# Kernel tuning notes

Measured on AMD Instinct MI355X. Metric: run time of the kernel, lower is better.

## Reference

```python
import jax, jax.numpy as jnp
import numpy as np

GRID = 33
STRIDE = 2
HIDDEN = 256
N_LAYERS = 4
BATCH = 64
N_NODES = GRID * GRID  # 1089


def _stride_edges(g, s):
    """Replicates StrideGraphSAGE.stride_edge (including the strict j > s test)."""
    idx = np.arange(g * g).reshape(g, g)
    srcs, dsts = [], []
    # right neighbor: j < g - s
    srcs.append(idx[:, : g - s].ravel()); dsts.append(idx[:, s:].ravel())
    # down neighbor: i < g - s
    srcs.append(idx[: g - s, :].ravel()); dsts.append(idx[s:, :].ravel())
    # down-right: j < g - s and i < g - s
    srcs.append(idx[: g - s, : g - s].ravel()); dsts.append(idx[s:, s:].ravel())
    # down-left: j > s and i < g - s  (strict >, as in the original)
    srcs.append(idx[: g - s, s + 1 :].ravel()); dsts.append(idx[s:, 1 : g - s].ravel())
    return (np.concatenate(srcs).astype(np.int32),
            np.concatenate(dsts).astype(np.int32))


def setup_inputs() -> dict:
    key = jax.random.key(0)
    kx, kwl, kbl, kwr = jax.random.split(key, 4)
    x = jax.random.normal(kx, (BATCH, HIDDEN, GRID, GRID), dtype=jnp.float32)
    Wl = jax.random.normal(kwl, (N_LAYERS, HIDDEN, HIDDEN), dtype=jnp.float32) * 0.05
    bl = jax.random.normal(kbl, (N_LAYERS, HIDDEN), dtype=jnp.float32) * 0.05
    Wr = jax.random.normal(kwr, (N_LAYERS, HIDDEN, HIDDEN), dtype=jnp.float32) * 0.05
    src_np, dst_np = _stride_edges(GRID, STRIDE)
    return {
        "x": x, "Wl": Wl, "bl": bl, "Wr": Wr,
        "src": jnp.asarray(src_np), "dst": jnp.asarray(dst_np),
    }


def reference(x, Wl, bl, Wr, src, dst):
    B, C, H, W = x.shape
    N = H * W
    total = B * N
    # feature2graph: each image -> [N, C] node matrix, then batched -> [B*N, C]
    nodes = x.reshape(B, C, N).transpose(0, 2, 1).reshape(total, C)

    # The original passes the UNOFFSET single-graph edge_index to every layer,
    # so messages only flow among the first N rows; the rest get zero aggregate.
    deg = jnp.zeros((total,), x.dtype).at[dst].add(1.0)
    inv_deg = jnp.where(deg > 0, 1.0 / jnp.maximum(deg, 1.0), 0.0)[:, None]

    L = Wl.shape[0]
    outs = []
    for l in range(L):
        # SAGEConv (mean aggr): lin_l(mean_j x_src_j) + lin_r(x) ; every layer
        # is applied to the ORIGINAL node features (x is never updated).
        agg = jnp.zeros_like(nodes).at[dst].add(nodes[src]) * inv_deg
        h = agg @ Wl[l] + bl[l] + nodes @ Wr[l]
        h = jax.nn.elu(h)
        # graph2feature: raw contiguous view [N, C] -> (C, H, W) per graph
        outs.append(h.reshape(B, C, H, W))
    outs.append(x)
    return jnp.concatenate(outs, axis=1)
```

## Files before the change

kernel.cpp:

```cpp
#include <hip/hip_runtime.h>
#include <hip/hip_bf16.h>
#include <stdint.h>


#define C_DIM 256
#define GRID_G 33
#define N_NODES 1089
#define BATCH 64
#define TOTAL (BATCH * N_NODES)
#define M_PAD 69760
#define CN (C_DIM * N_NODES)
#define OUT_STRIDE_B (5 * CN)
#define NCOLS 1024
#define AGG_ROWS_PAD 1280
#define MT 273
#define NWG (MT * 4)

using bf16 = __hip_bfloat16;
typedef __attribute__((ext_vector_type(8))) short short8;
typedef __attribute__((ext_vector_type(4))) float f32x4;

#define NODES_BYTES ((size_t)M_PAD * C_DIM * 2)
#define OFF_NODES   ((size_t)0)
#define OFF_AGGB    (NODES_BYTES)
#define AGGB_BYTES  ((size_t)AGG_ROWS_PAD * C_DIM * 2)
#define OFF_WLT     (OFF_AGGB + AGGB_BYTES)
#define WT_BYTES    ((size_t)NCOLS * C_DIM * 2)
#define OFF_WRT     (OFF_WLT + WT_BYTES)

__device__ __forceinline__ void gload16(void* lds, const void* g) {
    __builtin_amdgcn_global_load_lds(
        (const __attribute__((address_space(1))) uint32_t*)g,
        (__attribute__((address_space(3))) uint32_t*)lds,
        16, 0, 0);
}

__global__ __launch_bounds__(256)
void prep_kernel(const float* __restrict__ x,
                 const float* __restrict__ Wl, const float* __restrict__ Wr,
                 bf16* __restrict__ nodes, bf16* __restrict__ WlT, bf16* __restrict__ WrT,
                 float* __restrict__ out)
{
    __shared__ char smem[33792];
    const int t = threadIdx.x;
    const int bid = blockIdx.x;
    if (bid < 128) {
        float (*tile)[65] = (float(*)[65])smem;
        const int sel = bid & 1;
        const int l = (bid >> 1) & 3;
        const int kt = ((bid >> 3) & 3) * 64;
        const int ct = ((bid >> 5) & 3) * 64;
        const float* W = sel ? Wr : Wl;
        bf16* WT = sel ? WrT : WlT;
        const int tc = t & 63;
        const int tk = t >> 6;
#pragma unroll
        for (int i = 0; i < 16; ++i) {
            int kl = i * 4 + tk;
            tile[kl][tc] = W[((size_t)(l * 256 + kt + kl)) * 256 + ct + tc];
        }
        __syncthreads();
#pragma unroll
        for (int i = 0; i < 16; ++i) {
            int cl = i * 4 + tk;
            WT[((size_t)(l * 256 + ct + cl)) * 256 + kt + tc] = __float2bfloat16(tile[tc][cl]);
        }
    } else {
        bf16 (*tile)[66] = (bf16(*)[66])smem;
        const int bid2 = bid - 128;
        const int b = bid2 / 18;
        const int n0 = (bid2 % 18) * 64;
        const int nl = t & 63;
        const int cs = t >> 6;
        const int n = n0 + nl;
        const bool nvalid = n < N_NODES;
        const float* xb = x + (size_t)b * CN;
        float* outb = out + (size_t)b * OUT_STRIDE_B + (size_t)4 * CN;
#pragma unroll 4
        for (int cc = 0; cc < 64; ++cc) {
            int c = cc * 4 + cs;
            if (nvalid) {
                float v = xb[(size_t)c * N_NODES + n];
                outb[(size_t)c * N_NODES + n] = v;
                tile[c][nl] = __float2bfloat16(v);
            }
        }
        __syncthreads();
        const int half = t >> 7;
        const int c0 = (t & 127) * 2;
#pragma unroll
        for (int it = 0; it < 32; ++it) {
            int row = it * 2 + half;
            int nr = n0 + row;
            if (nr < N_NODES) {
                __hip_bfloat162 p;
                p.x = tile[c0][row];
                p.y = tile[c0 + 1][row];
                *(__hip_bfloat162*)(nodes + ((size_t)b * N_NODES + nr) * C_DIM + c0) = p;
            }
        }
    }
}

__global__ __launch_bounds__(256)
void gather_kernel(const bf16* __restrict__ nodes, bf16* __restrict__ aggb)
{
    const int n = blockIdx.x;
    const int c = threadIdx.x;
    if (n >= N_NODES) {
        aggb[(size_t)n * C_DIM + c] = __float2bfloat16(0.f);
        return;
    }
    const int i = n / GRID_G, j = n % GRID_G;
    float s = 0.f, d = 0.f;
    if (j >= 2)           { s += __bfloat162float(nodes[(size_t)(n - 2)  * C_DIM + c]); d += 1.f; }
    if (i >= 2)           { s += __bfloat162float(nodes[(size_t)(n - 66) * C_DIM + c]); d += 1.f; }
    if (i >= 2 && j >= 2) { s += __bfloat162float(nodes[(size_t)(n - 68) * C_DIM + c]); d += 1.f; }
    if (i >= 2 && j >= 1 && j <= 30)
                          { s += __bfloat162float(nodes[(size_t)(n - 64) * C_DIM + c]); d += 1.f; }
    aggb[(size_t)n * C_DIM + c] = __float2bfloat16(d > 0.f ? s / d : 0.f);
}

__global__ __launch_bounds__(512)
void gemm_kernel(const bf16* __restrict__ nodes, const bf16* __restrict__ agg,
                 const bf16* __restrict__ WrT, const bf16* __restrict__ WlT,
                 const float* __restrict__ bias, float* __restrict__ out)
{
    extern __shared__ char Sb[];
    const int t = threadIdx.x;
    const int lane = t & 63;
    const int w = t >> 6;
    const int wm = w >> 2;
    const int wn = w & 3;
    const int fr = lane & 15;
    const int kq = lane >> 4;

    const unsigned bid = blockIdx.x;
    const unsigned xcd = bid & 7, loc = bid >> 3;
    const unsigned swz = (xcd < 4 ? xcd * 137u : 4u * 137u + (xcd - 4u) * 136u) + loc;
    const int bcol = swz & 3;
    const int brow = swz >> 2;

    const int NT = (brow * 256 < N_NODES) ? 8 : 4;
    const size_t Arow0 = (size_t)brow * 256;
    const size_t Brow0 = (size_t)bcol * 256;

    f32x4 acc[8][4] = {};

    const int srow = t >> 3;
    const int sk = (((t & 7) ^ (srow & 7)) << 3);
    const int so0 = ((0 * 4 + kq) ^ (fr & 7)) << 4;
    const int so1 = ((1 * 4 + kq) ^ (fr & 7)) << 4;
    const int arow_b = (wm * 128 + fr) * 128;
    const int brow_b = (wn * 64 + fr) * 128;

    auto STAGE_HALF = [&](int kt, int half, int isB) {
        const int buf = kt & 1;
        const int kk0 = ((kt & 3) << 6) + sk;
        if (!isB) {
            const bf16* src = (kt < 4 ? nodes : agg);
            const size_t gr = Arow0 + half * 128 + srow;
            char* dst = Sb + buf * 32768 + half * 16384 + w * 1024;
            gload16(dst,        src + gr * 256 + kk0);
            gload16(dst + 8192, src + (gr + 64) * 256 + kk0);
        } else {
            const bf16* src = (kt < 4 ? WrT : WlT);
            const size_t gr = Brow0 + half * 128 + srow;
            char* dst = Sb + 65536 + buf * 32768 + half * 16384 + w * 1024;
            gload16(dst,        src + gr * 256 + kk0);
            gload16(dst + 8192, src + (gr + 64) * 256 + kk0);
        }
    };

    STAGE_HALF(0, 0, 0); STAGE_HALF(0, 1, 0); STAGE_HALF(0, 0, 1); STAGE_HALF(0, 1, 1);
    STAGE_HALF(1, 0, 0); STAGE_HALF(1, 1, 0); STAGE_HALF(1, 0, 1); STAGE_HALF(1, 1, 1);
    asm volatile("s_waitcnt vmcnt(8)" ::: "memory");
    __builtin_amdgcn_s_barrier();

    short8 av[4][2], bv0[2][2], bv1[2][2];

    for (int kt = 0; kt < NT; ++kt) {
        const int ab = (kt & 1) * 32768;
        const int bb = 65536 + (kt & 1) * 32768;
        const bool pf = (kt + 1 < NT);

#pragma unroll
        for (int i = 0; i < 4; ++i) {
            av[i][0] = *(const short8*)(Sb + ab + arow_b + i * 2048 + so0);
            av[i][1] = *(const short8*)(Sb + ab + arow_b + i * 2048 + so1);
        }
#pragma unroll
        for (int j = 0; j < 2; ++j) {
            bv0[j][0] = *(const short8*)(Sb + bb + brow_b + j * 2048 + so0);
            bv0[j][1] = *(const short8*)(Sb + bb + brow_b + j * 2048 + so1);
        }
        if (pf) STAGE_HALF(kt + 1, 0, 0);
        __builtin_amdgcn_s_barrier();
        asm volatile("s_waitcnt lgkmcnt(0)" ::: "memory");
        __builtin_amdgcn_sched_barrier(0);
        __builtin_amdgcn_s_setprio(1);
#pragma unroll
        for (int ks = 0; ks < 2; ++ks)
#pragma unroll
            for (int i = 0; i < 4; ++i)
#pragma unroll
                for (int j = 0; j < 2; ++j)
                    acc[i][j] = __builtin_amdgcn_mfma_f32_16x16x32_bf16(
                        av[i][ks], bv0[j][ks], acc[i][j], 0, 0, 0);
        __builtin_amdgcn_s_setprio(0);
        __builtin_amdgcn_s_barrier();

#pragma unroll
        for (int j = 0; j < 2; ++j) {
            bv1[j][0] = *(const short8*)(Sb + bb + brow_b + 4096 + j * 2048 + so0);
            bv1[j][1] = *(const short8*)(Sb + bb + brow_b + 4096 + j * 2048 + so1);
        }
        if (pf) STAGE_HALF(kt + 1, 1, 0);
        __builtin_amdgcn_s_barrier();
        asm volatile("s_waitcnt lgkmcnt(0)" ::: "memory");
        __builtin_amdgcn_sched_barrier(0);
        __builtin_amdgcn_s_setprio(1);
#pragma unroll
        for (int ks = 0; ks < 2; ++ks)
#pragma unroll
            for (int i = 0; i < 4; ++i)
#pragma unroll
                for (int j = 0; j < 2; ++j)
                    acc[i][2 + j] = __builtin_amdgcn_mfma_f32_16x16x32_bf16(
                        av[i][ks], bv1[j][ks], acc[i][2 + j], 0, 0, 0);
        __builtin_amdgcn_s_setprio(0);
        __builtin_amdgcn_s_barrier();

#pragma unroll
        for (int i = 0; i < 4; ++i) {
            av[i][0] = *(const short8*)(Sb + ab + arow_b + 8192 + i * 2048 + so0);
            av[i][1] = *(const short8*)(Sb + ab + arow_b + 8192 + i * 2048 + so1);
        }
        if (pf) STAGE_HALF(kt + 1, 0, 1);
        __builtin_amdgcn_s_barrier();
        asm volatile("s_waitcnt lgkmcnt(0)" ::: "memory");
        __builtin_amdgcn_sched_barrier(0);
        __builtin_amdgcn_s_setprio(1);
#pragma unroll
        for (int ks = 0; ks < 2; ++ks)
#pragma unroll
            for (int i = 0; i < 4; ++i)
#pragma unroll
                for (int j = 0; j < 2; ++j)
                    acc[4 + i][2 + j] = __builtin_amdgcn_mfma_f32_16x16x32_bf16(
                        av[i][ks], bv1[j][ks], acc[4 + i][2 + j], 0, 0, 0);
        __builtin_amdgcn_s_setprio(0);
        __builtin_amdgcn_s_barrier();

        if (pf) STAGE_HALF(kt + 1, 1, 1);
        __builtin_amdgcn_s_barrier();
        __builtin_amdgcn_s_setprio(1);
#pragma unroll
        for (int ks = 0; ks < 2; ++ks)
#pragma unroll
            for (int i = 0; i < 4; ++i)
#pragma unroll
                for (int j = 0; j < 2; ++j)
                    acc[4 + i][j] = __builtin_amdgcn_mfma_f32_16x16x32_bf16(
                        av[i][ks], bv0[j][ks], acc[4 + i][j], 0, 0, 0);
        __builtin_amdgcn_s_setprio(0);
        if (pf) asm volatile("s_waitcnt vmcnt(0)" ::: "memory");
        __builtin_amdgcn_s_barrier();
    }

    const int r0 = brow * 256 + wm * 128 + kq * 4;
    const unsigned bb0 = (unsigned)r0 / N_NODES;
    const int rsw = (int)((bb0 + 1) * N_NODES);
    float* outL = out + (size_t)bcol * CN;
    int cof[4];
    float bi[4];
#pragma unroll
    for (int nf = 0; nf < 4; ++nf) {
        int c = wn * 64 + nf * 16 + fr;
        cof[nf] = c;
        bi[nf] = bias[bcol * 256 + c];
    }
#pragma unroll
    for (int mf = 0; mf < 8; ++mf) {
#pragma unroll
        for (int reg = 0; reg < 4; ++reg) {
            int r = r0 + mf * 16 + reg;
            if (r < TOTAL) {
                int bb = (int)bb0 + (r >= rsw ? 1 : 0);
                int nn = r - bb * N_NODES;
                size_t base = (size_t)bb * OUT_STRIDE_B + (size_t)nn * C_DIM;
#pragma unroll
                for (int nf = 0; nf < 4; ++nf) {
                    float v = acc[mf][nf][reg] + bi[nf];
                    v = v > 0.f ? v : (__expf(v) - 1.0f);
                    outL[base + cof[nf]] = v;
                }
            }
        }
    }
}

extern "C" void kernel_launch(void* const* d_in, const int* in_sizes, int n_in,
                              void* d_out, int out_size, void* d_ws, size_t ws_size,
                              hipStream_t stream) {
    const float* x  = (const float*)d_in[0];
    const float* Wl = (const float*)d_in[1];
    const float* bl = (const float*)d_in[2];
    const float* Wr = (const float*)d_in[3];
    float* out = (float*)d_out;
    char* ws = (char*)d_ws;

    bf16* nodes = (bf16*)(ws + OFF_NODES);
    bf16* aggb  = (bf16*)(ws + OFF_AGGB);
    bf16* WlT   = (bf16*)(ws + OFF_WLT);
    bf16* WrT   = (bf16*)(ws + OFF_WRT);

    prep_kernel<<<128 + BATCH * 18, 256, 0, stream>>>(x, Wl, Wr, nodes, WlT, WrT, out);
    gather_kernel<<<AGG_ROWS_PAD, 256, 0, stream>>>(nodes, aggb);
    gemm_kernel<<<NWG, 512, 131072, stream>>>(nodes, aggb, WrT, WlT, bl, out);
}
```

Baseline: 159.8 us.

## Transpose MFMA operands for vectorized nontemporal epilogue stores and reorder tile schedule

Swaps the A/B operands of every MFMA so each lane holds four consecutive output columns, which lets the epilogue write 16-byte nontemporal f32x4 stores instead of scalar stores. Also switches the x passthrough copy to nontemporal stores. Remaps block rows so the heavier tiles (those that also include the aggregate K-range) are spread across XCDs and scheduled early. The aim is to cut output write traffic overhead and tail imbalance. The risk is that the remap or the nontemporal hints could hurt cache behavior.

```diff
diff --git a/kernel.cpp b/kernel.cpp
--- a/kernel.cpp
+++ b/kernel.cpp
@@ -81,7 +81,7 @@
             int c = cc * 4 + cs;
             if (nvalid) {
                 float v = xb[(size_t)c * N_NODES + n];
-                outb[(size_t)c * N_NODES + n] = v;
+                __builtin_nontemporal_store(v, &outb[(size_t)c * N_NODES + n]);
                 tile[c][nl] = __float2bfloat16(v);
             }
         }
@@ -139,7 +139,10 @@
     const unsigned xcd = bid & 7, loc = bid >> 3;
     const unsigned swz = (xcd < 4 ? xcd * 137u : 4u * 137u + (xcd - 4u) * 136u) + loc;
     const int bcol = swz & 3;
-    const int brow = swz >> 2;
+    int brow = (int)(swz >> 2);
+    if (brow >= 1 && brow <= 4) brow = brow * 34 + 1;
+    else if (brow >= 35 && brow <= 137 && ((brow - 1) % 34) == 0 && (brow - 1) / 34 <= 4)
+        brow = (brow - 1) / 34;
 
     const int NT = (brow * 256 < N_NODES) ? 8 : 4;
     const size_t Arow0 = (size_t)brow * 256;
@@ -206,7 +209,7 @@
 #pragma unroll
                 for (int j = 0; j < 2; ++j)
                     acc[i][j] = __builtin_amdgcn_mfma_f32_16x16x32_bf16(
-                        av[i][ks], bv0[j][ks], acc[i][j], 0, 0, 0);
+                        bv0[j][ks], av[i][ks], acc[i][j], 0, 0, 0);
         __builtin_amdgcn_s_setprio(0);
         __builtin_amdgcn_s_barrier();
 
@@ -227,7 +230,7 @@
 #pragma unroll
                 for (int j = 0; j < 2; ++j)
                     acc[i][2 + j] = __builtin_amdgcn_mfma_f32_16x16x32_bf16(
-                        av[i][ks], bv1[j][ks], acc[i][2 + j], 0, 0, 0);
+                        bv1[j][ks], av[i][ks], acc[i][2 + j], 0, 0, 0);
         __builtin_amdgcn_s_setprio(0);
         __builtin_amdgcn_s_barrier();
 
@@ -248,7 +251,7 @@
 #pragma unroll
                 for (int j = 0; j < 2; ++j)
                     acc[4 + i][2 + j] = __builtin_amdgcn_mfma_f32_16x16x32_bf16(
-                        av[i][ks], bv1[j][ks], acc[4 + i][2 + j], 0, 0, 0);
+                        bv1[j][ks], av[i][ks], acc[4 + i][2 + j], 0, 0, 0);
         __builtin_amdgcn_s_setprio(0);
         __builtin_amdgcn_s_barrier();
 
@@ -262,39 +265,36 @@
 #pragma unroll
                 for (int j = 0; j < 2; ++j)
                     acc[4 + i][j] = __builtin_amdgcn_mfma_f32_16x16x32_bf16(
-                        av[i][ks], bv0[j][ks], acc[4 + i][j], 0, 0, 0);
+                        bv0[j][ks], av[i][ks], acc[4 + i][j], 0, 0, 0);
         __builtin_amdgcn_s_setprio(0);
         if (pf) asm volatile("s_waitcnt vmcnt(0)" ::: "memory");
         __builtin_amdgcn_s_barrier();
     }
 
-    const int r0 = brow * 256 + wm * 128 + kq * 4;
+    const int r0 = brow * 256 + wm * 128 + fr;
     const unsigned bb0 = (unsigned)r0 / N_NODES;
     const int rsw = (int)((bb0 + 1) * N_NODES);
     float* outL = out + (size_t)bcol * CN;
-    int cof[4];
-    float bi[4];
-#pragma unroll
-    for (int nf = 0; nf < 4; ++nf) {
-        int c = wn * 64 + nf * 16 + fr;
-        cof[nf] = c;
-        bi[nf] = bias[bcol * 256 + c];
-    }
-#pragma unroll
-    for (int mf = 0; mf < 8; ++mf) {
-#pragma unroll
-        for (int reg = 0; reg < 4; ++reg) {
-            int r = r0 + mf * 16 + reg;
-            if (r < TOTAL) {
-                int bb = (int)bb0 + (r >= rsw ? 1 : 0);
-                int nn = r - bb * N_NODES;
-                size_t base = (size_t)bb * OUT_STRIDE_B + (size_t)nn * C_DIM;
-#pragma unroll
-                for (int nf = 0; nf < 4; ++nf) {
-                    float v = acc[mf][nf][reg] + bi[nf];
-                    v = v > 0.f ? v : (__expf(v) - 1.0f);
-                    outL[base + cof[nf]] = v;
-                }
+    const int cbase = wn * 64 + kq * 4;
+    f32x4 bi4[4];
+#pragma unroll
+    for (int J = 0; J < 4; ++J)
+        bi4[J] = *(const f32x4*)(bias + bcol * 256 + wn * 64 + J * 16 + kq * 4);
+#pragma unroll
+    for (int I = 0; I < 8; ++I) {
+        int r = r0 + I * 16;
+        if (r < TOTAL) {
+            int bb = (int)bb0 + (r >= rsw ? 1 : 0);
+            int nn = r - bb * N_NODES;
+            float* rowp = outL + (size_t)bb * OUT_STRIDE_B + (size_t)nn * C_DIM + cbase;
+#pragma unroll
+            for (int J = 0; J < 4; ++J) {
+                f32x4 v = acc[I][J] + bi4[J];
+                f32x4 o;
+#pragma unroll
+                for (int k = 0; k < 4; ++k)
+                    o[k] = v[k] > 0.f ? v[k] : (__expf(v[k]) - 1.0f);
+                __builtin_nontemporal_store(o, (f32x4*)(rowp + J * 16));
             }
         }
     }
```

New measurement: 161.1 us. Within noise of the previous version (+0.8%).
